# Kernel optimization log

Measured on AMD Instinct MI355X. Metric: run time of the kernel, lower is better.

The kernel has to match this reference:

```python
import jax, jax.numpy as jnp
import numpy as np

B, N, D, L = 4, 96, 512, 2
EPS = 1e-5


def setup_inputs() -> dict:
    key = jax.random.key(0)
    ks = jax.random.split(key, 8)
    s = 0.02  # weight init scale
    return {
        "node_feats": jax.random.normal(ks[0], (B, N, D), jnp.float32),
        "adj_mask": (jax.random.uniform(ks[1], (B, N, N)) < 0.5).astype(jnp.float32),
        # first Linear of each layer, split into hi-part and hj-part (in,out) layout
        "W1a": jax.random.normal(ks[2], (L, D, D), jnp.float32) * s,
        "W1b": jax.random.normal(ks[3], (L, D, D), jnp.float32) * s,
        "b1": jnp.zeros((L, D), jnp.float32),
        "W2": jax.random.normal(ks[4], (L, D, D), jnp.float32) * s,
        "b2": jnp.zeros((L, D), jnp.float32),
        "gamma": jnp.ones((D,), jnp.float32),
        "beta": jnp.zeros((D,), jnp.float32),
    }


def _layer_norm(x, gamma, beta):
    mu = x.mean(-1, keepdims=True)
    var = ((x - mu) ** 2).mean(-1, keepdims=True)  # biased, as torch LayerNorm
    return (x - mu) * jax.lax.rsqrt(var + EPS) * gamma + beta


def reference(node_feats, adj_mask, W1a, W1b, b1, W2, b2, gamma, beta):
    h = node_feats  # (B,N,D)
    n_layers = W1a.shape[0]
    inv_n = 1.0 / h.shape[1]
    for l in range(n_layers):
        # Linear1 on cat([hi,hj]) == hi@W1a + hj@W1b + b1 (same math, no (B,N,N,2D))
        a = jnp.einsum('bnd,de->bne', h, W1a[l])  # hi projection
        b = jnp.einsum('bnd,de->bne', h, W1b[l])  # hj projection
        z = jax.nn.relu(a[:, :, None, :] + b[:, None, :, :] + b1[l])  # (B,N,N,D)
        m = jnp.einsum('bijd,de->bije', z, W2[l]) + b2[l]
        m = m * adj_mask[..., None]
        msg = m.sum(axis=2) * inv_n  # mean over j
        h = _layer_norm(h + msg, gamma, beta)  # dropout is identity in eval
    return jnp.clip(h, -100.0, 100.0)
```

## Files before the change

kernel.cpp:

```cpp
#include <hip/hip_runtime.h>

#define DD 512
#define NNODE 96
#define NBATCH 4
#define MROWS (NBATCH * NNODE)
#define EPSF 1e-5f
#define INVN (1.0f / 96.0f)

typedef short short8v __attribute__((ext_vector_type(8)));
typedef float f32x4   __attribute__((ext_vector_type(4)));

static __device__ __forceinline__ unsigned short f2bf(float x) {
    union { float f; unsigned int u; } v; v.f = x;
    unsigned int r = v.u + 0x7fffu + ((v.u >> 16) & 1u);
    return (unsigned short)(r >> 16);
}

__global__ __launch_bounds__(256) void convert_w(
    const float* __restrict__ W1a, const float* __restrict__ W1b,
    const float* __restrict__ W2, const float* __restrict__ h0,
    unsigned short* __restrict__ WT, unsigned short* __restrict__ Hbf)
{
    const int tx = threadIdx.x, ty = threadIdx.y;
    const int z = blockIdx.z;
    const int c0 = blockIdx.x * 32, r0 = blockIdx.y * 32;

    if (z == 6) {
        if (r0 >= MROWS) return;
#pragma unroll
        for (int i = 0; i < 4; ++i) {
            const int r = r0 + ty + 8 * i;
            Hbf[(size_t)r * DD + c0 + tx] = f2bf(h0[(size_t)r * DD + c0 + tx]);
        }
        return;
    }

    __shared__ float t[32][33];
    const int l = z / 3, w = z % 3;
    const float* __restrict__ src =
        (w == 0 ? W1a : (w == 1 ? W1b : W2)) + (size_t)l * DD * DD;
    unsigned short* __restrict__ dst = WT + (size_t)z * DD * DD;

#pragma unroll
    for (int i = 0; i < 4; ++i)
        t[ty + 8 * i][tx] = src[(size_t)(r0 + ty + 8 * i) * DD + c0 + tx];
    __syncthreads();
#pragma unroll
    for (int i = 0; i < 4; ++i)
        dst[(size_t)(c0 + ty + 8 * i) * DD + r0 + tx] = f2bf(t[tx][ty + 8 * i]);
}

__global__ __launch_bounds__(256) void gemm_ab(
    const unsigned short* __restrict__ Xbf,
    const unsigned short* __restrict__ WaT,
    const unsigned short* __restrict__ WbT,
    const float* __restrict__ b1,
    float* __restrict__ outA, float* __restrict__ outB)
{
    const int lane = threadIdx.x & 63;
    const int wv   = threadIdx.x >> 6;
    const int m0   = (blockIdx.x * 4 + wv) * 16;
    const int n0   = blockIdx.y * 16;
    const int isB  = blockIdx.z;
    const unsigned short* __restrict__ Wt = isB ? WbT : WaT;

    const int lo = lane & 15, hi = lane >> 4;
    const unsigned short* ap = Xbf + (size_t)(m0 + lo) * DD + 8 * hi;
    const unsigned short* bp = Wt  + (size_t)(n0 + lo) * DD + 8 * hi;

    f32x4 acc = {0.f, 0.f, 0.f, 0.f};
#pragma unroll 4
    for (int k0 = 0; k0 < DD; k0 += 32) {
        const short8v a = *(const short8v*)(ap + k0);
        const short8v b = *(const short8v*)(bp + k0);
        acc = __builtin_amdgcn_mfma_f32_16x16x32_bf16(a, b, acc, 0, 0, 0);
    }

    const int col = n0 + lo;
    const float bias = isB ? 0.f : b1[col];
    float* __restrict__ outp = isB ? outB : outA;
    const int rb = m0 + 4 * hi;
#pragma unroll
    for (int i = 0; i < 4; ++i)
        outp[(size_t)(rb + i) * DD + col] = acc[i] + bias;
}

__global__ __launch_bounds__(64) void relusum(
    const float* __restrict__ a, const float* __restrict__ bb,
    const float* __restrict__ mask, unsigned short* __restrict__ s,
    float* __restrict__ cnt)
{
    const int b   = blockIdx.x;
    const int i0  = blockIdx.y * 4;
    const int d   = blockIdx.z * 64 + threadIdx.x;
    const int tid = threadIdx.x;

    __shared__ float mk[4][96];
    for (int t = tid; t < 4 * 96; t += 64)
        mk[t / 96][t % 96] = mask[(size_t)(b * 96 + i0 + t / 96) * 96 + (t % 96)];
    __syncthreads();

    const float* arow = a + (size_t)(b * 96 + i0) * DD + d;
    const float a0 = arow[0], a1 = arow[DD], a2 = arow[2 * DD], a3 = arow[3 * DD];
    float s0 = 0.f, s1 = 0.f, s2 = 0.f, s3 = 0.f;

    const float* brow = bb + (size_t)b * 96 * DD + d;
#pragma unroll 8
    for (int j = 0; j < 96; ++j) {
        const float bv = brow[(size_t)j * DD];
        s0 = fmaf(mk[0][j], fmaxf(a0 + bv, 0.f), s0);
        s1 = fmaf(mk[1][j], fmaxf(a1 + bv, 0.f), s1);
        s2 = fmaf(mk[2][j], fmaxf(a2 + bv, 0.f), s2);
        s3 = fmaf(mk[3][j], fmaxf(a3 + bv, 0.f), s3);
    }

    unsigned short* srow = s + (size_t)(b * 96 + i0) * DD + d;
    srow[0]      = f2bf(s0);
    srow[DD]     = f2bf(s1);
    srow[2 * DD] = f2bf(s2);
    srow[3 * DD] = f2bf(s3);

    if (blockIdx.z == 0 && tid < 4) {
        float c = 0.f;
        for (int j = 0; j < 96; ++j) c += mk[tid][j];
        cnt[b * 96 + i0 + tid] = c;
    }
}

__global__ __launch_bounds__(256) void gemm_msg(
    const unsigned short* __restrict__ Sbf,
    const unsigned short* __restrict__ W2T,
    const float* __restrict__ b2, const float* __restrict__ cnt,
    const float* __restrict__ hin, float* __restrict__ U)
{
    const int lane = threadIdx.x & 63;
    const int wv   = threadIdx.x >> 6;
    const int m0   = (blockIdx.x * 4 + wv) * 16;
    const int n0   = blockIdx.y * 16;

    const int lo = lane & 15, hi = lane >> 4;
    const unsigned short* ap = Sbf + (size_t)(m0 + lo) * DD + 8 * hi;
    const unsigned short* bp = W2T + (size_t)(n0 + lo) * DD + 8 * hi;

    f32x4 acc = {0.f, 0.f, 0.f, 0.f};
#pragma unroll 4
    for (int k0 = 0; k0 < DD; k0 += 32) {
        const short8v a = *(const short8v*)(ap + k0);
        const short8v b = *(const short8v*)(bp + k0);
        acc = __builtin_amdgcn_mfma_f32_16x16x32_bf16(a, b, acc, 0, 0, 0);
    }

    const int col = n0 + lo;
    const float b2c = b2[col];
    const int rb = m0 + 4 * hi;
#pragma unroll
    for (int i = 0; i < 4; ++i) {
        const int r = rb + i;
        U[(size_t)r * DD + col] =
            hin[(size_t)r * DD + col] + INVN * acc[i] + (cnt[r] * INVN) * b2c;
    }
}

__global__ __launch_bounds__(128) void layer_norm(
    const float* __restrict__ u, const float* __restrict__ gamma,
    const float* __restrict__ beta, float* __restrict__ out,
    unsigned short* __restrict__ out_bf, int doClip)
{
    const int r   = blockIdx.x;
    const int tid = threadIdx.x;
    const float4 x = *(const float4*)&u[(size_t)r * DD + tid * 4];

    float s = x.x + x.y + x.z + x.w;
#pragma unroll
    for (int off = 32; off > 0; off >>= 1) s += __shfl_xor(s, off);

    __shared__ float red[2];
    __shared__ float red2[2];
    const int wid = tid >> 6;
    if ((tid & 63) == 0) red[wid] = s;
    __syncthreads();
    const float mu = (red[0] + red[1]) * (1.0f / 512.0f);

    const float dx = x.x - mu, dy = x.y - mu, dz = x.z - mu, dw = x.w - mu;
    float q = dx * dx + dy * dy + dz * dz + dw * dw;
#pragma unroll
    for (int off = 32; off > 0; off >>= 1) q += __shfl_xor(q, off);
    if ((tid & 63) == 0) red2[wid] = q;
    __syncthreads();
    const float var = (red2[0] + red2[1]) * (1.0f / 512.0f);
    const float rs  = rsqrtf(var + EPSF);

    const float4 g  = *(const float4*)&gamma[tid * 4];
    const float4 bt = *(const float4*)&beta[tid * 4];
    float4 y;
    y.x = dx * rs * g.x + bt.x;
    y.y = dy * rs * g.y + bt.y;
    y.z = dz * rs * g.z + bt.z;
    y.w = dw * rs * g.w + bt.w;
    if (doClip) {
        y.x = fminf(fmaxf(y.x, -100.f), 100.f);
        y.y = fminf(fmaxf(y.y, -100.f), 100.f);
        y.z = fminf(fmaxf(y.z, -100.f), 100.f);
        y.w = fminf(fmaxf(y.w, -100.f), 100.f);
    }
    *(float4*)&out[(size_t)r * DD + tid * 4] = y;

    if (out_bf) {
        uint2 p;
        p.x = (unsigned int)f2bf(y.x) | ((unsigned int)f2bf(y.y) << 16);
        p.y = (unsigned int)f2bf(y.z) | ((unsigned int)f2bf(y.w) << 16);
        *(uint2*)&out_bf[(size_t)r * DD + tid * 4] = p;
    }
}

extern "C" void kernel_launch(void* const* d_in, const int* in_sizes, int n_in,
                              void* d_out, int out_size, void* d_ws, size_t ws_size,
                              hipStream_t stream)
{
    const float* h0    = (const float*)d_in[0];
    const float* adj   = (const float*)d_in[1];
    const float* W1a   = (const float*)d_in[2];
    const float* W1b   = (const float*)d_in[3];
    const float* b1    = (const float*)d_in[4];
    const float* W2    = (const float*)d_in[5];
    const float* b2    = (const float*)d_in[6];
    const float* gamma = (const float*)d_in[7];
    const float* beta  = (const float*)d_in[8];
    float* out = (float*)d_out;

    char* p = (char*)d_ws;
    unsigned short* WT  = (unsigned short*)p;  p += 6u * DD * DD * 2;
    unsigned short* Hbf = (unsigned short*)p;  p += MROWS * DD * 2;
    unsigned short* Sbf = (unsigned short*)p;  p += MROWS * DD * 2;
    float* A   = (float*)p;  p += MROWS * DD * 4;
    float* Bb  = (float*)p;  p += MROWS * DD * 4;
    float* H1  = (float*)p;  p += MROWS * DD * 4;
    float* CNT = (float*)p;

    convert_w<<<dim3(16, 16, 7), dim3(32, 8), 0, stream>>>(W1a, W1b, W2, h0, WT, Hbf);

    for (int l = 0; l < 2; ++l) {
        const unsigned short* waT = WT + (size_t)(l * 3 + 0) * DD * DD;
        const unsigned short* wbT = WT + (size_t)(l * 3 + 1) * DD * DD;
        const unsigned short* w2T = WT + (size_t)(l * 3 + 2) * DD * DD;
        const float* bb1 = b1 + (size_t)l * DD;
        const float* bb2 = b2 + (size_t)l * DD;
        const float* hin = (l == 0) ? h0 : H1;
        float* hout = (l == 0) ? H1 : out;
        unsigned short* hbf_out = (l == 0) ? Hbf : nullptr;

        gemm_ab<<<dim3(6, 32, 2), 256, 0, stream>>>(Hbf, waT, wbT, bb1, A, Bb);
        relusum<<<dim3(4, 24, 8), 64, 0, stream>>>(A, Bb, adj, Sbf, CNT);
        gemm_msg<<<dim3(6, 32), 256, 0, stream>>>(Sbf, w2T, bb2, CNT, hin, A );
        layer_norm<<<dim3(384), 128, 0, stream>>>(A , gamma, beta, hout,
                                                  hbf_out, l == 1);
    }
}
```

Before: 63.02 us.

## Fuse projection GEMMs with relu-sum, and message GEMM with layernorm

The hi/hj projection GEMMs are merged with the masked relu-sum into one per-batch kernel. Each block computes a 96x32 slab of both projections into LDS, keeps the batch's adjacency mask in shared memory, and writes the bf16 sum directly. The W2 GEMM, residual, bias and layernorm are fused into a second kernel that stages 16 rows in LDS. The neighbour-count reduction moves into the initial conversion kernel. Together these cut launches per layer from four to two and remove the fp32 A/B/U intermediates in global memory. In exchange the grids are much smaller (64 and 24 blocks), which may leave most CUs idle and serialise more MFMA work per wave.

```diff
diff --git a/kernel.cpp b/kernel.cpp
--- a/kernel.cpp
+++ b/kernel.cpp
@@ -1,9 +1,7 @@
 #include <hip/hip_runtime.h>
 
 #define DD 512
-#define NNODE 96
-#define NBATCH 4
-#define MROWS (NBATCH * NNODE)
+#define MROWS 384
 #define EPSF 1e-5f
 #define INVN (1.0f / 96.0f)
 
@@ -16,21 +14,38 @@
     return (unsigned short)(r >> 16);
 }
 
-__global__ __launch_bounds__(256) void convert_w(
+__global__ __launch_bounds__(256) void convert_all(
     const float* __restrict__ W1a, const float* __restrict__ W1b,
     const float* __restrict__ W2, const float* __restrict__ h0,
-    unsigned short* __restrict__ WT, unsigned short* __restrict__ Hbf)
+    const float* __restrict__ adj,
+    unsigned short* __restrict__ WT, unsigned short* __restrict__ Hbf,
+    float* __restrict__ CNT)
 {
     const int tx = threadIdx.x, ty = threadIdx.y;
-    const int z = blockIdx.z;
+    const int z  = blockIdx.z;
     const int c0 = blockIdx.x * 32, r0 = blockIdx.y * 32;
 
     if (z == 6) {
-        if (r0 >= MROWS) return;
-#pragma unroll
-        for (int i = 0; i < 4; ++i) {
-            const int r = r0 + ty + 8 * i;
-            Hbf[(size_t)r * DD + c0 + tx] = f2bf(h0[(size_t)r * DD + c0 + tx]);
+        if (blockIdx.y < 12) {
+#pragma unroll
+            for (int i = 0; i < 4; ++i) {
+                const int r = r0 + ty + 8 * i;
+                Hbf[(size_t)r * DD + c0 + tx] = f2bf(h0[(size_t)r * DD + c0 + tx]);
+            }
+        } else if (blockIdx.y == 12) {
+            const int tid  = ty * 32 + tx;
+            const int lane = tid & 63;
+            const int wv   = tid >> 6;
+            const int rb   = (blockIdx.x * 4 + wv) * 6;
+#pragma unroll
+            for (int q = 0; q < 6; ++q) {
+                const float* mrow = adj + (size_t)(rb + q) * 96;
+                float v = mrow[lane];
+                if (lane < 32) v += mrow[64 + lane];
+#pragma unroll
+                for (int off = 32; off > 0; off >>= 1) v += __shfl_xor(v, off);
+                if (lane == 0) CNT[rb + q] = v;
+            }
         }
         return;
     }
@@ -50,166 +65,150 @@
         dst[(size_t)(c0 + ty + 8 * i) * DD + r0 + tx] = f2bf(t[tx][ty + 8 * i]);
 }
 
-__global__ __launch_bounds__(256) void gemm_ab(
-    const unsigned short* __restrict__ Xbf,
+__global__ __launch_bounds__(512) void layer_front(
+    const unsigned short* __restrict__ Hbf,
     const unsigned short* __restrict__ WaT,
     const unsigned short* __restrict__ WbT,
-    const float* __restrict__ b1,
-    float* __restrict__ outA, float* __restrict__ outB)
-{
-    const int lane = threadIdx.x & 63;
-    const int wv   = threadIdx.x >> 6;
-    const int m0   = (blockIdx.x * 4 + wv) * 16;
-    const int n0   = blockIdx.y * 16;
-    const int isB  = blockIdx.z;
+    const float* __restrict__ b1l, const float* __restrict__ adj,
+    unsigned short* __restrict__ Sbf)
+{
+    __shared__ float As[96][32];
+    __shared__ float Bs[96][32];
+    __shared__ float msh[96][96];
+
+    const int tid = threadIdx.x;
+    const int b   = blockIdx.x;
+    const int d0  = blockIdx.y * 32;
+
+    const float* __restrict__ ab = adj + (size_t)b * 96 * 96;
+#pragma unroll
+    for (int s = 0; s < 18; ++s) {
+        const int t = tid + s * 512;
+        msh[t / 96][t % 96] = ab[t];
+    }
+
+    const int lane = tid & 63;
+    const int wv   = tid >> 6;
+    const int lo = lane & 15, hi = lane >> 4;
+    const int isB  = wv >= 4;
     const unsigned short* __restrict__ Wt = isB ? WbT : WaT;
-
-    const int lo = lane & 15, hi = lane >> 4;
-    const unsigned short* ap = Xbf + (size_t)(m0 + lo) * DD + 8 * hi;
-    const unsigned short* bp = Wt  + (size_t)(n0 + lo) * DD + 8 * hi;
-
-    f32x4 acc = {0.f, 0.f, 0.f, 0.f};
+    float (* __restrict__ dst)[32] = isB ? Bs : As;
+
+    for (int i = 0; i < 3; ++i) {
+        const int tt = (wv & 3) * 3 + i;
+        const int mt = tt % 6;
+        const int nt = tt / 6;
+        const unsigned short* ap = Hbf + (size_t)(b * 96 + mt * 16 + lo) * DD + 8 * hi;
+        const unsigned short* bp = Wt  + (size_t)(d0 + nt * 16 + lo) * DD + 8 * hi;
+        f32x4 acc = {0.f, 0.f, 0.f, 0.f};
+#pragma unroll
+        for (int k0 = 0; k0 < DD; k0 += 32)
+            acc = __builtin_amdgcn_mfma_f32_16x16x32_bf16(
+                *(const short8v*)(ap + k0), *(const short8v*)(bp + k0), acc, 0, 0, 0);
+        const int cl = nt * 16 + lo;
+        const float bias = isB ? 0.f : b1l[d0 + cl];
+        const int rb = mt * 16 + 4 * hi;
+#pragma unroll
+        for (int q = 0; q < 4; ++q)
+            dst[rb + q][cl] = acc[q] + bias;
+    }
+    __syncthreads();
+
+    const int dd = tid & 31;
+    const int i0 = (tid >> 5) * 6;
+    float a6[6], s6[6];
+#pragma unroll
+    for (int q = 0; q < 6; ++q) { a6[q] = As[i0 + q][dd]; s6[q] = 0.f; }
 #pragma unroll 4
-    for (int k0 = 0; k0 < DD; k0 += 32) {
-        const short8v a = *(const short8v*)(ap + k0);
-        const short8v b = *(const short8v*)(bp + k0);
-        acc = __builtin_amdgcn_mfma_f32_16x16x32_bf16(a, b, acc, 0, 0, 0);
-    }
-
-    const int col = n0 + lo;
-    const float bias = isB ? 0.f : b1[col];
-    float* __restrict__ outp = isB ? outB : outA;
-    const int rb = m0 + 4 * hi;
-#pragma unroll
-    for (int i = 0; i < 4; ++i)
-        outp[(size_t)(rb + i) * DD + col] = acc[i] + bias;
-}
-
-__global__ __launch_bounds__(64) void relusum(
-    const float* __restrict__ a, const float* __restrict__ bb,
-    const float* __restrict__ mask, unsigned short* __restrict__ s,
-    float* __restrict__ cnt)
-{
-    const int b   = blockIdx.x;
-    const int i0  = blockIdx.y * 4;
-    const int d   = blockIdx.z * 64 + threadIdx.x;
-    const int tid = threadIdx.x;
-
-    __shared__ float mk[4][96];
-    for (int t = tid; t < 4 * 96; t += 64)
-        mk[t / 96][t % 96] = mask[(size_t)(b * 96 + i0 + t / 96) * 96 + (t % 96)];
-    __syncthreads();
-
-    const float* arow = a + (size_t)(b * 96 + i0) * DD + d;
-    const float a0 = arow[0], a1 = arow[DD], a2 = arow[2 * DD], a3 = arow[3 * DD];
-    float s0 = 0.f, s1 = 0.f, s2 = 0.f, s3 = 0.f;
-
-    const float* brow = bb + (size_t)b * 96 * DD + d;
-#pragma unroll 8
     for (int j = 0; j < 96; ++j) {
-        const float bv = brow[(size_t)j * DD];
-        s0 = fmaf(mk[0][j], fmaxf(a0 + bv, 0.f), s0);
-        s1 = fmaf(mk[1][j], fmaxf(a1 + bv, 0.f), s1);
-        s2 = fmaf(mk[2][j], fmaxf(a2 + bv, 0.f), s2);
-        s3 = fmaf(mk[3][j], fmaxf(a3 + bv, 0.f), s3);
-    }
-
-    unsigned short* srow = s + (size_t)(b * 96 + i0) * DD + d;
-    srow[0]      = f2bf(s0);
-    srow[DD]     = f2bf(s1);
-    srow[2 * DD] = f2bf(s2);
-    srow[3 * DD] = f2bf(s3);
-
-    if (blockIdx.z == 0 && tid < 4) {
-        float c = 0.f;
-        for (int j = 0; j < 96; ++j) c += mk[tid][j];
-        cnt[b * 96 + i0 + tid] = c;
-    }
-}
-
-__global__ __launch_bounds__(256) void gemm_msg(
+        const float bv = Bs[j][dd];
+#pragma unroll
+        for (int q = 0; q < 6; ++q)
+            s6[q] = fmaf(msh[i0 + q][j], fmaxf(a6[q] + bv, 0.f), s6[q]);
+    }
+#pragma unroll
+    for (int q = 0; q < 6; ++q)
+        Sbf[(size_t)(b * 96 + i0 + q) * DD + d0 + dd] = f2bf(s6[q]);
+}
+
+__global__ __launch_bounds__(512) void layer_back(
     const unsigned short* __restrict__ Sbf,
     const unsigned short* __restrict__ W2T,
-    const float* __restrict__ b2, const float* __restrict__ cnt,
-    const float* __restrict__ hin, float* __restrict__ U)
-{
-    const int lane = threadIdx.x & 63;
-    const int wv   = threadIdx.x >> 6;
-    const int m0   = (blockIdx.x * 4 + wv) * 16;
-    const int n0   = blockIdx.y * 16;
-
+    const float* __restrict__ b2l, const float* __restrict__ cnt,
+    const float* __restrict__ hin, const float* __restrict__ gamma,
+    const float* __restrict__ beta, float* __restrict__ hout,
+    unsigned short* __restrict__ hbf_out, int doClip)
+{
+    __shared__ float Us[16][512];
+
+    const int tid  = threadIdx.x;
+    const int m0   = blockIdx.x * 16;
+    const int lane = tid & 63;
+    const int wv   = tid >> 6;
     const int lo = lane & 15, hi = lane >> 4;
-    const unsigned short* ap = Sbf + (size_t)(m0 + lo) * DD + 8 * hi;
-    const unsigned short* bp = W2T + (size_t)(n0 + lo) * DD + 8 * hi;
-
-    f32x4 acc = {0.f, 0.f, 0.f, 0.f};
-#pragma unroll 4
-    for (int k0 = 0; k0 < DD; k0 += 32) {
-        const short8v a = *(const short8v*)(ap + k0);
-        const short8v b = *(const short8v*)(bp + k0);
-        acc = __builtin_amdgcn_mfma_f32_16x16x32_bf16(a, b, acc, 0, 0, 0);
-    }
-
-    const int col = n0 + lo;
-    const float b2c = b2[col];
-    const int rb = m0 + 4 * hi;
-#pragma unroll
+
     for (int i = 0; i < 4; ++i) {
-        const int r = rb + i;
-        U[(size_t)r * DD + col] =
-            hin[(size_t)r * DD + col] + INVN * acc[i] + (cnt[r] * INVN) * b2c;
-    }
-}
-
-__global__ __launch_bounds__(128) void layer_norm(
-    const float* __restrict__ u, const float* __restrict__ gamma,
-    const float* __restrict__ beta, float* __restrict__ out,
-    unsigned short* __restrict__ out_bf, int doClip)
-{
-    const int r   = blockIdx.x;
-    const int tid = threadIdx.x;
-    const float4 x = *(const float4*)&u[(size_t)r * DD + tid * 4];
-
-    float s = x.x + x.y + x.z + x.w;
-#pragma unroll
-    for (int off = 32; off > 0; off >>= 1) s += __shfl_xor(s, off);
-
-    __shared__ float red[2];
-    __shared__ float red2[2];
-    const int wid = tid >> 6;
-    if ((tid & 63) == 0) red[wid] = s;
+        const int n0 = (wv * 4 + i) * 16;
+        const unsigned short* ap = Sbf + (size_t)(m0 + lo) * DD + 8 * hi;
+        const unsigned short* bp = W2T + (size_t)(n0 + lo) * DD + 8 * hi;
+        f32x4 acc = {0.f, 0.f, 0.f, 0.f};
+#pragma unroll
+        for (int k0 = 0; k0 < DD; k0 += 32)
+            acc = __builtin_amdgcn_mfma_f32_16x16x32_bf16(
+                *(const short8v*)(ap + k0), *(const short8v*)(bp + k0), acc, 0, 0, 0);
+        const int col = n0 + lo;
+        const float b2c = b2l[col];
+#pragma unroll
+        for (int q = 0; q < 4; ++q) {
+            const int rr = 4 * hi + q;
+            const int r  = m0 + rr;
+            Us[rr][col] = hin[(size_t)r * DD + col] + INVN * acc[q]
+                        + (cnt[r] * INVN) * b2c;
+        }
+    }
     __syncthreads();
-    const float mu = (red[0] + red[1]) * (1.0f / 512.0f);
-
-    const float dx = x.x - mu, dy = x.y - mu, dz = x.z - mu, dw = x.w - mu;
-    float q = dx * dx + dy * dy + dz * dz + dw * dw;
-#pragma unroll
-    for (int off = 32; off > 0; off >>= 1) q += __shfl_xor(q, off);
-    if ((tid & 63) == 0) red2[wid] = q;
-    __syncthreads();
-    const float var = (red2[0] + red2[1]) * (1.0f / 512.0f);
-    const float rs  = rsqrtf(var + EPSF);
-
-    const float4 g  = *(const float4*)&gamma[tid * 4];
-    const float4 bt = *(const float4*)&beta[tid * 4];
-    float4 y;
-    y.x = dx * rs * g.x + bt.x;
-    y.y = dy * rs * g.y + bt.y;
-    y.z = dz * rs * g.z + bt.z;
-    y.w = dw * rs * g.w + bt.w;
-    if (doClip) {
-        y.x = fminf(fmaxf(y.x, -100.f), 100.f);
-        y.y = fminf(fmaxf(y.y, -100.f), 100.f);
-        y.z = fminf(fmaxf(y.z, -100.f), 100.f);
-        y.w = fminf(fmaxf(y.w, -100.f), 100.f);
-    }
-    *(float4*)&out[(size_t)r * DD + tid * 4] = y;
-
-    if (out_bf) {
-        uint2 p;
-        p.x = (unsigned int)f2bf(y.x) | ((unsigned int)f2bf(y.y) << 16);
-        p.y = (unsigned int)f2bf(y.z) | ((unsigned int)f2bf(y.w) << 16);
-        *(uint2*)&out_bf[(size_t)r * DD + tid * 4] = p;
+
+#pragma unroll
+    for (int rr = wv * 2; rr <= wv * 2 + 1; ++rr) {
+        const int r = m0 + rr;
+        const float4 x0 = *(const float4*)&Us[rr][lane * 8];
+        const float4 x1 = *(const float4*)&Us[rr][lane * 8 + 4];
+        float s = x0.x + x0.y + x0.z + x0.w + x1.x + x1.y + x1.z + x1.w;
+#pragma unroll
+        for (int off = 32; off > 0; off >>= 1) s += __shfl_xor(s, off);
+        const float mu = s * (1.0f / 512.0f);
+        const float d0 = x0.x - mu, d1 = x0.y - mu, d2 = x0.z - mu, d3 = x0.w - mu;
+        const float d4 = x1.x - mu, d5 = x1.y - mu, d6 = x1.z - mu, d7 = x1.w - mu;
+        float q = d0*d0 + d1*d1 + d2*d2 + d3*d3 + d4*d4 + d5*d5 + d6*d6 + d7*d7;
+#pragma unroll
+        for (int off = 32; off > 0; off >>= 1) q += __shfl_xor(q, off);
+        const float rs = rsqrtf(q * (1.0f / 512.0f) + EPSF);
+
+        const float4 g0 = *(const float4*)(gamma + lane * 8);
+        const float4 g1 = *(const float4*)(gamma + lane * 8 + 4);
+        const float4 t0 = *(const float4*)(beta + lane * 8);
+        const float4 t1 = *(const float4*)(beta + lane * 8 + 4);
+        float y0 = d0*rs*g0.x + t0.x, y1 = d1*rs*g0.y + t0.y;
+        float y2 = d2*rs*g0.z + t0.z, y3 = d3*rs*g0.w + t0.w;
+        float y4 = d4*rs*g1.x + t1.x, y5 = d5*rs*g1.y + t1.y;
+        float y6 = d6*rs*g1.z + t1.z, y7 = d7*rs*g1.w + t1.w;
+        if (doClip) {
+            y0 = fminf(fmaxf(y0, -100.f), 100.f); y1 = fminf(fmaxf(y1, -100.f), 100.f);
+            y2 = fminf(fmaxf(y2, -100.f), 100.f); y3 = fminf(fmaxf(y3, -100.f), 100.f);
+            y4 = fminf(fmaxf(y4, -100.f), 100.f); y5 = fminf(fmaxf(y5, -100.f), 100.f);
+            y6 = fminf(fmaxf(y6, -100.f), 100.f); y7 = fminf(fmaxf(y7, -100.f), 100.f);
+        }
+        float4 o0 = {y0, y1, y2, y3}, o1 = {y4, y5, y6, y7};
+        *(float4*)(hout + (size_t)r * DD + lane * 8)     = o0;
+        *(float4*)(hout + (size_t)r * DD + lane * 8 + 4) = o1;
+        if (hbf_out) {
+            uint4 u;
+            u.x = (unsigned)f2bf(y0) | ((unsigned)f2bf(y1) << 16);
+            u.y = (unsigned)f2bf(y2) | ((unsigned)f2bf(y3) << 16);
+            u.z = (unsigned)f2bf(y4) | ((unsigned)f2bf(y5) << 16);
+            u.w = (unsigned)f2bf(y6) | ((unsigned)f2bf(y7) << 16);
+            *(uint4*)(hbf_out + (size_t)r * DD + lane * 8) = u;
+        }
     }
 }
 
@@ -232,27 +231,24 @@
     unsigned short* WT  = (unsigned short*)p;  p += 6u * DD * DD * 2;
     unsigned short* Hbf = (unsigned short*)p;  p += MROWS * DD * 2;
     unsigned short* Sbf = (unsigned short*)p;  p += MROWS * DD * 2;
-    float* A   = (float*)p;  p += MROWS * DD * 4;
-    float* Bb  = (float*)p;  p += MROWS * DD * 4;
     float* H1  = (float*)p;  p += MROWS * DD * 4;
     float* CNT = (float*)p;
 
-    convert_w<<<dim3(16, 16, 7), dim3(32, 8), 0, stream>>>(W1a, W1b, W2, h0, WT, Hbf);
+    convert_all<<<dim3(16, 16, 7), dim3(32, 8), 0, stream>>>(
+        W1a, W1b, W2, h0, adj, WT, Hbf, CNT);
 
     for (int l = 0; l < 2; ++l) {
         const unsigned short* waT = WT + (size_t)(l * 3 + 0) * DD * DD;
         const unsigned short* wbT = WT + (size_t)(l * 3 + 1) * DD * DD;
         const unsigned short* w2T = WT + (size_t)(l * 3 + 2) * DD * DD;
-        const float* bb1 = b1 + (size_t)l * DD;
-        const float* bb2 = b2 + (size_t)l * DD;
         const float* hin = (l == 0) ? h0 : H1;
         float* hout = (l == 0) ? H1 : out;
-        unsigned short* hbf_out = (l == 0) ? Hbf : nullptr;
-
-        gemm_ab<<<dim3(6, 32, 2), 256, 0, stream>>>(Hbf, waT, wbT, bb1, A, Bb);
-        relusum<<<dim3(4, 24, 8), 64, 0, stream>>>(A, Bb, adj, Sbf, CNT);
-        gemm_msg<<<dim3(6, 32), 256, 0, stream>>>(Sbf, w2T, bb2, CNT, hin, A );
-        layer_norm<<<dim3(384), 128, 0, stream>>>(A , gamma, beta, hout,
-                                                  hbf_out, l == 1);
-    }
-}
+        unsigned short* hbf_next = (l == 0) ? Hbf : nullptr;
+
+        layer_front<<<dim3(4, 16), 512, 0, stream>>>(
+            Hbf, waT, wbT, b1 + (size_t)l * DD, adj, Sbf);
+        layer_back<<<dim3(24), 512, 0, stream>>>(
+            Sbf, w2T, b2 + (size_t)l * DD, CNT, hin, gamma, beta, hout,
+            hbf_next, l == 1);
+    }
+}
```

New measurement: 118.9 us. 88.7% more time.
